# Kernel optimization log

Hardware: AMD Instinct MI355X
Metric: run time of the kernel (lower is better)

Reference implementation:

```python
import jax, jax.numpy as jnp
import numpy as np

B, C, H, W = 2, 320, 48, 48
HEADS, DIM_HEAD, NUM_FILTERS = 8, 64, 32
INNER = HEADS * DIM_HEAD  # 512
LN_EPS = 1e-05


def setup_inputs() -> dict:
    key = jax.random.key(0)
    ks = jax.random.split(key, 8)
    w = 0.02
    return {
        "hidden_states": jax.random.normal(ks[0], (B, C, H, W), jnp.float32),
        "encoder_hidden_states": jax.random.normal(ks[1], (B, C, H, W), jnp.float32),
        "Wq": jax.random.normal(ks[2], (C, INNER), jnp.float32) * w,
        "Wk": jax.random.normal(ks[3], (C, INNER), jnp.float32) * w,
        "Wv": jax.random.normal(ks[4], (C, INNER), jnp.float32) * w,
        "Wo": jax.random.normal(ks[5], (INNER, C), jnp.float32) * w,
        "bo": jnp.zeros((C,), jnp.float32),
        "ln_gamma": jnp.ones((C,), jnp.float32),
        "ln_beta": jnp.zeros((C,), jnp.float32),
        "ex_filters": jax.random.normal(ks[6], (NUM_FILTERS, INNER), jnp.float32),
        "dist_filters": jax.random.normal(ks[7], (NUM_FILTERS, INNER), jnp.float32),
        "scale": jnp.ones((1,), jnp.float32),  # learnable scale shadows dim_head**-0.5
    }


def _split_heads(t, heads):
    b, s, d = t.shape
    return t.reshape(b, s, heads, d // heads).transpose(0, 2, 1, 3)  # [b,h,s,dh]


def reference(hidden_states, encoder_hidden_states, Wq, Wk, Wv, Wo, bo,
              ln_gamma, ln_beta, ex_filters, dist_filters, scale):
    b, c, h, w = hidden_states.shape
    _, _, rh, rw = encoder_hidden_states.shape
    residual = hidden_states
    s = scale[0]

    hs = hidden_states.transpose(0, 2, 3, 1).reshape(b, h * w, c)        # [b, q, C]
    ehs = encoder_hidden_states.transpose(0, 2, 3, 1).reshape(b, rh * rw, c)

    # LayerNorm on encoder states
    mu = ehs.mean(-1, keepdims=True)
    var = jnp.mean((ehs - mu) ** 2, axis=-1, keepdims=True)
    ehs = (ehs - mu) * jax.lax.rsqrt(var + LN_EPS) * ln_gamma + ln_beta

    q = _split_heads(hs @ Wq, HEADS)    # [b,h,q,dh]
    k = _split_heads(ehs @ Wk, HEADS)   # [b,h,kv,dh]
    v = _split_heads(ehs @ Wv, HEADS)   # [b,h,kv,dh]
    ef = _split_heads(jnp.broadcast_to(ex_filters[None], (b,) + ex_filters.shape), HEADS)   # [b,h,F,dh]
    df = _split_heads(jnp.broadcast_to(dist_filters[None], (b,) + dist_filters.shape), HEADS)

    # spatial attention: softmax over kv positions
    spatial = jax.nn.softmax(jnp.einsum('bhfd,bhkd->bhfk', ef, k) * s, axis=-1)   # [b,h,F,kv]
    # channel attention: softmax over the filter axis (torch dim=1 of [B*h, F, q])
    channel = jax.nn.softmax(jnp.einsum('bhfd,bhqd->bhfq', df, q) * s, axis=2)    # [b,h,F,q]

    attn = jnp.einsum('bhfq,bhfk->bhqk', channel, spatial)                        # [b,h,q,kv]
    out = jnp.einsum('bhqk,bhkd->bhqd', attn, v)                                  # [b,h,q,dh]

    out = out.transpose(0, 2, 1, 3).reshape(b, h * w, INNER)
    out = out @ Wo + bo
    out = out.reshape(b, h, w, c).transpose(0, 3, 1, 2)
    return out + residual * s
```

## Files before the change

### kernel.cpp

```cpp
#include <hip/hip_runtime.h>
#include <math.h>

#define Bc 2
#define Cc 320
#define Pc 2304
#define HEADSc 8
#define DHc 64
#define INNERc 512
#define Fc 32
#define LN_EPS 1e-5f
#define CHUNKS 36
#define CHUNK_P 64

typedef __attribute__((ext_vector_type(8))) short bf16x8;
typedef __attribute__((ext_vector_type(4))) float f32x4;

static __device__ __forceinline__ ushort f2bf(float x) {
  uint u = __builtin_bit_cast(uint, x);
  u = (u + 0x7fffu + ((u >> 16) & 1u)) >> 16;
  return (ushort)u;
}

static __device__ __forceinline__ void gload16(const ushort* g, ushort* l) {
  __builtin_amdgcn_global_load_lds(
      (const __attribute__((address_space(1))) uint*)g,
      (__attribute__((address_space(3))) uint*)l, 16, 0, 0);
}

static __device__ void transpose_tile(const float* __restrict__ src,
                                      ushort* __restrict__ dst, int R, int C,
                                      int r0, int c0, int tid,
                                      float (*t)[65]) {
#pragma unroll
  for (int it = 0; it < 4; ++it) {
    int lin = it * 256 + tid;
    int rr = lin >> 4, c4 = lin & 15;
    float4 v = *(const float4*)(&src[(size_t)(r0 + rr) * C + c0 + c4 * 4]);
    t[rr][c4 * 4 + 0] = v.x; t[rr][c4 * 4 + 1] = v.y;
    t[rr][c4 * 4 + 2] = v.z; t[rr][c4 * 4 + 3] = v.w;
  }
  __syncthreads();
#pragma unroll
  for (int it = 0; it < 2; ++it) {
    int lin = it * 256 + tid;
    int cc = lin >> 3, r8 = lin & 7;
    ushort tmp[8];
#pragma unroll
    for (int j = 0; j < 8; ++j) tmp[j] = f2bf(t[r8 * 8 + j][cc]);
    *(uint4*)(&dst[(size_t)(c0 + cc) * R + r0 + r8 * 8]) = *(const uint4*)tmp;
  }
}

__global__ __launch_bounds__(256) void prep_all_kernel(
    const float* __restrict__ hs, const float* __restrict__ ehs,
    const float* __restrict__ gamma, const float* __restrict__ beta,
    const float* __restrict__ Wv, const float* __restrict__ Wo,
    const float* __restrict__ exf, const float* __restrict__ Wk,
    const float* __restrict__ dif, const float* __restrict__ Wq,
    ushort* __restrict__ hsT, ushort* __restrict__ ehsT,
    ushort* __restrict__ WvT, ushort* __restrict__ WoT,
    ushort* __restrict__ Gk, ushort* __restrict__ Gq) {
  __shared__ float smem[6448];
  int idx = blockIdx.x, tid = threadIdx.x;

  if (idx < 144) {
    int pt = idx % 36, z = idx / 36;
    int b = z & 1, which = z >> 1;
    int pos0 = pt * 64;
    const float* src = (which ? ehs : hs) + (size_t)b * Cc * Pc;
    ushort* dst = (which ? ehsT : hsT) + (size_t)b * Pc * Cc;
    float* t = smem;
    float* s1 = smem + 4160;
    float* s2 = smem + 4416;
    float* lmean = smem + 4672;
    float* lrstd = smem + 4736;
    int lane = tid & 63, g = tid >> 6;
    if (which) {
      const float* base = src + pos0 + lane;
      float sum = 0.f, sq = 0.f;
      for (int c = g * 80; c < g * 80 + 80; ++c) {
        float x = base[(size_t)c * Pc];
        sum += x; sq += x * x;
      }
      s1[g * 64 + lane] = sum; s2[g * 64 + lane] = sq;
      __syncthreads();
      if (tid < 64) {
        float ts = s1[tid] + s1[64 + tid] + s1[128 + tid] + s1[192 + tid];
        float tq = s2[tid] + s2[64 + tid] + s2[128 + tid] + s2[192 + tid];
        float mean = ts / (float)Cc;
        float var = tq / (float)Cc - mean * mean;
        lmean[tid] = mean;
        lrstd[tid] = rsqrtf(var + LN_EPS);
      }
      __syncthreads();
    }
    for (int ct = 0; ct < 5; ++ct) {
      int r0 = ct * 64;
#pragma unroll
      for (int it = 0; it < 4; ++it) {
        int lin = it * 256 + tid;
        int rr = lin >> 4, c4 = lin & 15;
        float4 v = *(const float4*)(&src[(size_t)(r0 + rr) * Pc + pos0 + c4 * 4]);
        t[rr * 65 + c4 * 4 + 0] = v.x; t[rr * 65 + c4 * 4 + 1] = v.y;
        t[rr * 65 + c4 * 4 + 2] = v.z; t[rr * 65 + c4 * 4 + 3] = v.w;
      }
      __syncthreads();
#pragma unroll
      for (int it = 0; it < 2; ++it) {
        int lin = it * 256 + tid;
        int cc = lin >> 3, r8 = lin & 7;
        float m_ = which ? lmean[cc] : 0.f, rs_ = which ? lrstd[cc] : 1.f;
        ushort tmp[8];
#pragma unroll
        for (int j = 0; j < 8; ++j) {
          int ch = r8 * 8 + j;
          float x = t[ch * 65 + cc];
          float val = which ? (x - m_) * rs_ * gamma[r0 + ch] + beta[r0 + ch] : x;
          tmp[j] = f2bf(val);
        }
        *(uint4*)(&dst[(size_t)(pos0 + cc) * Cc + r0 + r8 * 8]) =
            *(const uint4*)tmp;
      }
      __syncthreads();
    }
  } else {
    int idx2 = idx - 144;
    if (idx2 < 40) {
      transpose_tile(Wv, WvT, Cc, INNERc, (idx2 / 8) * 64, (idx2 % 8) * 64,
                     tid, (float(*)[65])smem);
    } else if (idx2 < 80) {
      int i = idx2 - 40;
      transpose_tile(Wo, WoT, INNERc, Cc, (i / 5) * 64, (i % 5) * 64, tid,
                     (float(*)[65])smem);
    } else {
      int i = idx2 - 80;
      int c0 = (i % 5) * 64, h = (i / 5) % 8, zz = i / 40;
      const float* filt = zz ? dif : exf;
      const float* W = zz ? Wq : Wk;
      ushort* G = zz ? Gq : Gk;
      float (*ef)[66] = (float(*)[66])smem;
      float (*wk)[65] = (float(*)[65])(smem + 32 * 66);
      for (int l = tid; l < Fc * DHc; l += 256) {
        int f = l >> 6, d = l & 63;
        ef[f][d] = filt[(size_t)f * INNERc + h * 64 + d];
      }
      for (int l = tid; l < 64 * DHc; l += 256) {
        int cc = l >> 6, d = l & 63;
        wk[cc][d] = W[(size_t)(c0 + cc) * INNERc + h * 64 + d];
      }
      __syncthreads();
      int f = tid >> 3, cbase = tid & 7;
      float acc[8] = {};
#pragma unroll
      for (int d4 = 0; d4 < DHc; d4 += 4) {
        float4 a = *(const float4*)(&ef[f][d4]);
#pragma unroll
        for (int j = 0; j < 8; ++j) {
          float4 b = *(const float4*)(&wk[cbase + j * 8][d4]);
          acc[j] += a.x * b.x + a.y * b.y + a.z * b.z + a.w * b.w;
        }
      }
#pragma unroll
      for (int j = 0; j < 8; ++j)
        G[(size_t)(h * Fc + f) * Cc + c0 + cbase + j * 8] = f2bf(acc[j]);
    }
  }
}

__global__ __launch_bounds__(256) void spatial_kernel(
    const ushort* __restrict__ Gk, const ushort* __restrict__ ehsT,
    const ushort* __restrict__ WvT, const float* __restrict__ scale_p,
    float* __restrict__ svp, float* __restrict__ mj, float* __restrict__ lj) {
  int c = blockIdx.x, h = blockIdx.y, b = blockIdx.z;
  int tid = threadIdx.x, lane = tid & 63, wv = tid >> 6;
  int l15 = lane & 15, kq = lane >> 4;
  int pos0 = c * CHUNK_P;
  int bh = b * HEADSc + h;
  float s = scale_p[0];

  __shared__ alignas(16) char smem[22528];
  ushort* As = (ushort*)smem;
  ushort* Bs = (ushort*)(smem + 12288);
  float* Sq = (float*)smem;
  ushort* Vs = (ushort*)(smem + 8704);
  ushort* P = (ushort*)(smem + 17920);

  const ushort* Av = WvT + (size_t)(h * 64) * Cc;
  const ushort* Ag = Gk + (size_t)(h * Fc) * Cc;
  const ushort* Bb = ehsT + ((size_t)b * Pc + pos0) * Cc;

  f32x4 acc[6] = {};
  for (int k0 = 0; k0 < Cc; k0 += 64) {
#pragma unroll
    for (int it = 0; it < 3; ++it) {
      int lin = it * 256 + tid;
      int row = lin >> 3, p = lin & 7;
      int lc = p ^ (row & 7);
      const ushort* sp = (row < 64) ? (Av + (size_t)row * Cc + k0 + lc * 8)
                                    : (Ag + (size_t)(row - 64) * Cc + k0 + lc * 8);
      gload16(sp, &As[lin * 8]);
    }
#pragma unroll
    for (int it = 0; it < 2; ++it) {
      int lin = it * 256 + tid;
      int row = lin >> 3, p = lin & 7;
      int lc = p ^ (row & 7);
      gload16(Bb + (size_t)row * Cc + k0 + lc * 8, &Bs[lin * 8]);
    }
    __syncthreads();
#pragma unroll
    for (int ss = 0; ss < 2; ++ss) {
      bf16x8 af[6], bfr;
#pragma unroll
      for (int mt = 0; mt < 6; ++mt) {
        int m = mt * 16 + l15;
        int p = (ss * 4 + kq) ^ (m & 7);
        af[mt] = *(const bf16x8*)(&As[m * 64 + p * 8]);
      }
      {
        int n = wv * 16 + l15;
        int p = (ss * 4 + kq) ^ (n & 7);
        bfr = *(const bf16x8*)(&Bs[n * 64 + p * 8]);
      }
#pragma unroll
      for (int mt = 0; mt < 6; ++mt)
        acc[mt] = __builtin_amdgcn_mfma_f32_16x16x32_bf16(af[mt], bfr, acc[mt],
                                                          0, 0, 0);
    }
    __syncthreads();
  }
#pragma unroll
  for (int mt = 0; mt < 6; ++mt) {
    int col = wv * 16 + l15;
#pragma unroll
    for (int r = 0; r < 4; ++r) {
      int row = mt * 16 + kq * 4 + r;
      if (mt < 4) Vs[row * 72 + col] = f2bf(acc[mt][r]);
      else Sq[(row - 64) * 68 + col] = acc[mt][r];
    }
  }
  __syncthreads();

  {
    int row = tid >> 3, sub = tid & 7;
    float vals[8];
    float m_ = -1e30f;
#pragma unroll
    for (int i = 0; i < 8; ++i) {
      vals[i] = s * Sq[row * 68 + sub * 8 + i];
      m_ = fmaxf(m_, vals[i]);
    }
    m_ = fmaxf(m_, __shfl_xor(m_, 1));
    m_ = fmaxf(m_, __shfl_xor(m_, 2));
    m_ = fmaxf(m_, __shfl_xor(m_, 4));
    float l_ = 0.f;
#pragma unroll
    for (int i = 0; i < 8; i += 2) {
      float e0 = __expf(vals[i] - m_);
      float e1 = __expf(vals[i + 1] - m_);
      l_ += e0 + e1;
      uint pk = (uint)f2bf(e0) | ((uint)f2bf(e1) << 16);
      *(uint*)(&P[row * 72 + sub * 8 + i]) = pk;
    }
    l_ += __shfl_xor(l_, 1);
    l_ += __shfl_xor(l_, 2);
    l_ += __shfl_xor(l_, 4);
    if (sub == 0) {
      mj[((size_t)c * 16 + bh) * Fc + row] = m_;
      lj[((size_t)c * 16 + bh) * Fc + row] = l_;
    }
  }
  __syncthreads();

  f32x4 acc2[2] = {};
#pragma unroll
  for (int ss = 0; ss < 2; ++ss) {
    bf16x8 af[2];
#pragma unroll
    for (int mt = 0; mt < 2; ++mt)
      af[mt] = *(const bf16x8*)(&P[(mt * 16 + l15) * 72 + ss * 32 + kq * 8]);
    bf16x8 bfr = *(const bf16x8*)(&Vs[(wv * 16 + l15) * 72 + ss * 32 + kq * 8]);
#pragma unroll
    for (int mt = 0; mt < 2; ++mt)
      acc2[mt] = __builtin_amdgcn_mfma_f32_16x16x32_bf16(af[mt], bfr, acc2[mt],
                                                         0, 0, 0);
  }
  float* op = svp + ((size_t)c * 16 + bh) * (Fc * DHc);
#pragma unroll
  for (int mt = 0; mt < 2; ++mt)
#pragma unroll
    for (int r = 0; r < 4; ++r)
      op[(mt * 16 + kq * 4 + r) * DHc + wv * 16 + l15] = acc2[mt][r];
}

__global__ __launch_bounds__(256) void sv_reduce_kernel(
    const float* __restrict__ svp, const float* __restrict__ mj,
    const float* __restrict__ lj, ushort* __restrict__ svT) {
  int idx = blockIdx.x * 256 + threadIdx.x;
  int d = idx & 63, fr = idx >> 6;
  int bh = fr >> 5, f = fr & 31;
  float m = -1e30f;
#pragma unroll
  for (int c = 0; c < CHUNKS; ++c)
    m = fmaxf(m, mj[((size_t)c * 16 + bh) * Fc + f]);
  float osum = 0.f, lsum = 0.f;
#pragma unroll 4
  for (int c = 0; c < CHUNKS; ++c) {
    float w = __expf(mj[((size_t)c * 16 + bh) * Fc + f] - m);
    osum += w * svp[((size_t)c * 16 + bh) * (Fc * DHc) + f * DHc + d];
    lsum += w * lj[((size_t)c * 16 + bh) * Fc + f];
  }
  svT[((size_t)bh * DHc + d) * Fc + f] = f2bf(osum / lsum);
}

__global__ __launch_bounds__(256) void channel_kernel(
    const ushort* __restrict__ Gq, const ushort* __restrict__ hsT,
    const ushort* __restrict__ svT, const float* __restrict__ scale_p,
    ushort* __restrict__ OAT) {
  int pb = blockIdx.x, h = blockIdx.y, b = blockIdx.z;
  int pos0 = pb * 64;
  int tid = threadIdx.x, lane = tid & 63, wv = tid >> 6;
  int l15 = lane & 15, kq = lane >> 4;
  float s = scale_p[0];

  __shared__ alignas(16) char smem[28672];
  ushort* Aq = (ushort*)smem;
  ushort* Bs = (ushort*)(smem + 4096);
  float* SO = (float*)smem;
  ushort* Pt = (ushort*)(smem + 17408);
  ushort* svs = (ushort*)(smem + 22528);
  float* red = (float*)(smem + 27648);

  f32x4 acc[2] = {};
  const ushort* Bb = hsT + ((size_t)b * Pc + pos0) * Cc;
  const ushort* Ab = Gq + (size_t)(h * Fc) * Cc;
  for (int k0 = 0; k0 < Cc; k0 += 64) {
    {
      int lin = tid;
      int row = lin >> 3, p = lin & 7;
      int lc = p ^ (row & 7);
      gload16(Ab + (size_t)row * Cc + k0 + lc * 8, &Aq[lin * 8]);
    }
#pragma unroll
    for (int it = 0; it < 2; ++it) {
      int lin = it * 256 + tid;
      int row = lin >> 3, p = lin & 7;
      int lc = p ^ (row & 7);
      gload16(Bb + (size_t)row * Cc + k0 + lc * 8, &Bs[lin * 8]);
    }
    __syncthreads();
#pragma unroll
    for (int ss = 0; ss < 2; ++ss) {
      int n = wv * 16 + l15;
      int pb_ = (ss * 4 + kq) ^ (n & 7);
      bf16x8 bfr = *(const bf16x8*)(&Bs[n * 64 + pb_ * 8]);
#pragma unroll
      for (int mt = 0; mt < 2; ++mt) {
        int m = mt * 16 + l15;
        int pa = (ss * 4 + kq) ^ (m & 7);
        bf16x8 af = *(const bf16x8*)(&Aq[m * 64 + pa * 8]);
        acc[mt] = __builtin_amdgcn_mfma_f32_16x16x32_bf16(af, bfr, acc[mt],
                                                          0, 0, 0);
      }
    }
    __syncthreads();
  }

#pragma unroll
  for (int mt = 0; mt < 2; ++mt)
#pragma unroll
    for (int r = 0; r < 4; ++r)
      SO[(mt * 16 + kq * 4 + r) * 68 + wv * 16 + l15] = acc[mt][r];
  {
    int rr = tid >> 2, p = tid & 3;
    *(uint4*)(&svs[rr * 40 + p * 8]) = *(const uint4*)(
        svT + ((size_t)(b * HEADSc + h) * DHc + rr) * Fc + p * 8);
  }
  __syncthreads();
  {
    int pos = tid & 63, g = tid >> 6;
    float v8[8];
    float pm = -1e30f;
#pragma unroll
    for (int i = 0; i < 8; ++i) {
      v8[i] = s * SO[(g * 8 + i) * 68 + pos];
      pm = fmaxf(pm, v8[i]);
    }
    red[g * 64 + pos] = pm;
    __syncthreads();
    float m_ = fmaxf(fmaxf(red[pos], red[64 + pos]),
                     fmaxf(red[128 + pos], red[192 + pos]));
    __syncthreads();
    float ps = 0.f;
#pragma unroll
    for (int i = 0; i < 8; ++i) {
      v8[i] = __expf(v8[i] - m_);
      ps += v8[i];
    }
    red[g * 64 + pos] = ps;
    __syncthreads();
    float inv = 1.f / (red[pos] + red[64 + pos] + red[128 + pos] +
                       red[192 + pos]);
#pragma unroll
    for (int i = 0; i < 8; i += 2) {
      uint pk = (uint)f2bf(v8[i] * inv) | ((uint)f2bf(v8[i + 1] * inv) << 16);
      *(uint*)(&Pt[pos * 40 + g * 8 + i]) = pk;
    }
  }
  __syncthreads();
  {
    bf16x8 b_ = *(const bf16x8*)(&svs[(wv * 16 + l15) * 40 + kq * 8]);
    f32x4 acc3[4];
#pragma unroll
    for (int mt = 0; mt < 4; ++mt) {
      bf16x8 a_ = *(const bf16x8*)(&Pt[(mt * 16 + l15) * 40 + kq * 8]);
      f32x4 z = {0.f, 0.f, 0.f, 0.f};
      acc3[mt] = __builtin_amdgcn_mfma_f32_16x16x32_bf16(a_, b_, z, 0, 0, 0);
    }
#pragma unroll
    for (int mt = 0; mt < 4; ++mt)
#pragma unroll
      for (int r = 0; r < 4; ++r)
        SO[(mt * 16 + kq * 4 + r) * 68 + wv * 16 + l15] = acc3[mt][r];
  }
  __syncthreads();
#pragma unroll
  for (int it = 0; it < 2; ++it) {
    int lin = it * 256 + tid;
    int p = lin >> 3, c8 = lin & 7;
    ushort tmp[8];
#pragma unroll
    for (int j = 0; j < 8; ++j) tmp[j] = f2bf(SO[p * 68 + c8 * 8 + j]);
    *(uint4*)(&OAT[((size_t)b * Pc + pos0 + p) * INNERc + h * 64 + c8 * 8]) =
        *(const uint4*)tmp;
  }
}

__global__ __launch_bounds__(256) void gemm_mfma_kernel(
    const ushort* __restrict__ A, const ushort* __restrict__ Bt,
    float* __restrict__ Out, int K, int Mdim,
    const float* __restrict__ bias, const float* __restrict__ res,
    const float* __restrict__ scale_p) {
  int b = blockIdx.z;
  int n0 = blockIdx.x * 64, m0 = blockIdx.y * 64;
  int tid = threadIdx.x, lane = tid & 63, wv = tid >> 6;
  int l15 = lane & 15, kq = lane >> 4;
  __shared__ alignas(16) ushort As[64 * 64];
  __shared__ alignas(16) ushort Bs[64 * 64];
  const ushort* Ab = A + (size_t)m0 * K;
  const ushort* Bb = Bt + ((size_t)b * Pc + n0) * K;

  f32x4 acc[4] = {};
  for (int k0 = 0; k0 < K; k0 += 64) {
#pragma unroll
    for (int it = 0; it < 2; ++it) {
      int lin = it * 256 + tid;
      int row = lin >> 3, p = lin & 7;
      int lc = p ^ (row & 7);
      gload16(Ab + (size_t)row * K + k0 + lc * 8, &As[lin * 8]);
    }
#pragma unroll
    for (int it = 0; it < 2; ++it) {
      int lin = it * 256 + tid;
      int row = lin >> 3, p = lin & 7;
      int lc = p ^ (row & 7);
      gload16(Bb + (size_t)row * K + k0 + lc * 8, &Bs[lin * 8]);
    }
    __syncthreads();
#pragma unroll
    for (int ss = 0; ss < 2; ++ss) {
      bf16x8 af[4], bfr;
#pragma unroll
      for (int mt = 0; mt < 4; ++mt) {
        int m = mt * 16 + l15;
        int p = (ss * 4 + kq) ^ (m & 7);
        af[mt] = *(const bf16x8*)(&As[m * 64 + p * 8]);
      }
      {
        int n = wv * 16 + l15;
        int p = (ss * 4 + kq) ^ (n & 7);
        bfr = *(const bf16x8*)(&Bs[n * 64 + p * 8]);
      }
#pragma unroll
      for (int mt = 0; mt < 4; ++mt)
        acc[mt] = __builtin_amdgcn_mfma_f32_16x16x32_bf16(af[mt], bfr, acc[mt],
                                                          0, 0, 0);
    }
    __syncthreads();
  }
  float s = scale_p[0];
  float* Ob = Out + ((size_t)b * Mdim + m0) * Pc + n0;
  const float* rb = res + ((size_t)b * Mdim + m0) * Pc + n0;
  int ncol = wv * 16 + l15;
#pragma unroll
  for (int mt = 0; mt < 4; ++mt)
#pragma unroll
    for (int r = 0; r < 4; ++r) {
      int m = mt * 16 + kq * 4 + r;
      Ob[(size_t)m * Pc + ncol] =
          acc[mt][r] + bias[m0 + m] + s * rb[(size_t)m * Pc + ncol];
    }
}

extern "C" void kernel_launch(void* const* d_in, const int* in_sizes, int n_in,
                              void* d_out, int out_size, void* d_ws, size_t ws_size,
                              hipStream_t stream) {
  const float* hs    = (const float*)d_in[0];
  const float* ehs   = (const float*)d_in[1];
  const float* Wq    = (const float*)d_in[2];
  const float* Wk    = (const float*)d_in[3];
  const float* Wv    = (const float*)d_in[4];
  const float* Wo    = (const float*)d_in[5];
  const float* bo    = (const float*)d_in[6];
  const float* gamma = (const float*)d_in[7];
  const float* beta  = (const float*)d_in[8];
  const float* exf   = (const float*)d_in[9];
  const float* dif   = (const float*)d_in[10];
  const float* scale = (const float*)d_in[11];
  float* out = (float*)d_out;

  float* ws = (float*)d_ws;
  float* svp = ws;
  float* mj  = svp + 1179648;
  float* lj  = mj + 18432;
  ushort* hsT  = (ushort*)(lj + 18432);
  ushort* ehsT = hsT + 1474560;
  ushort* WvT  = ehsT + 1474560;
  ushort* WoT  = WvT + 163840;
  ushort* Gk   = WoT + 163840;
  ushort* Gq   = Gk + 81920;
  ushort* svT  = Gq + 81920;
  ushort* OAT  = svT + 32768;

  prep_all_kernel<<<dim3(304), dim3(256), 0, stream>>>(
      hs, ehs, gamma, beta, Wv, Wo, exf, Wk, dif, Wq,
      hsT, ehsT, WvT, WoT, Gk, Gq);
  spatial_kernel<<<dim3(CHUNKS, HEADSc, Bc), dim3(256), 0, stream>>>(
      Gk, ehsT, WvT, scale, svp, mj, lj);
  sv_reduce_kernel<<<dim3(128), dim3(256), 0, stream>>>(svp, mj, lj, svT);
  channel_kernel<<<dim3(Pc / 64, HEADSc, Bc), dim3(256), 0, stream>>>(
      Gq, hsT, svT, scale, OAT);
  gemm_mfma_kernel<<<dim3(Pc / 64, Cc / 64, Bc), dim3(256), 0, stream>>>(
      WoT, OAT, out, INNERc, Cc, bo, hs, scale);
}
```

Baseline: 133.2 us.

## Double-buffer LDS tiles in MFMA GEMM kernels and prefetch transpose loads

Adds two-stage LDS double buffering to the spatial, channel and output-projection GEMM kernels, so the next K tile's async global-to-LDS loads are issued before the current tile's MFMAs run. The transpose/layernorm prep kernel also prefetches the next 64-channel slab into registers while the current slab is written out. The aim is to hide global memory latency behind compute. In exchange it raises LDS use (spatial kernel grows to 40KB), which may cut occupancy. The mid-loop barrier is removed, so correctness relies on the async LDS loads having completed by the trailing __syncthreads.

```diff
diff --git a/kernel.cpp b/kernel.cpp
--- a/kernel.cpp
+++ b/kernel.cpp
@@ -94,17 +94,31 @@
       }
       __syncthreads();
     }
+    float4 pv[4];
+#pragma unroll
+    for (int it = 0; it < 4; ++it) {
+      int lin = it * 256 + tid, rr = lin >> 4, c4 = lin & 15;
+      pv[it] = *(const float4*)(&src[(size_t)rr * Pc + pos0 + c4 * 4]);
+    }
     for (int ct = 0; ct < 5; ++ct) {
       int r0 = ct * 64;
 #pragma unroll
       for (int it = 0; it < 4; ++it) {
-        int lin = it * 256 + tid;
-        int rr = lin >> 4, c4 = lin & 15;
-        float4 v = *(const float4*)(&src[(size_t)(r0 + rr) * Pc + pos0 + c4 * 4]);
-        t[rr * 65 + c4 * 4 + 0] = v.x; t[rr * 65 + c4 * 4 + 1] = v.y;
-        t[rr * 65 + c4 * 4 + 2] = v.z; t[rr * 65 + c4 * 4 + 3] = v.w;
+        int lin = it * 256 + tid, rr = lin >> 4, c4 = lin & 15;
+        t[rr * 65 + c4 * 4 + 0] = pv[it].x;
+        t[rr * 65 + c4 * 4 + 1] = pv[it].y;
+        t[rr * 65 + c4 * 4 + 2] = pv[it].z;
+        t[rr * 65 + c4 * 4 + 3] = pv[it].w;
       }
       __syncthreads();
+      if (ct < 4) {
+#pragma unroll
+        for (int it = 0; it < 4; ++it) {
+          int lin = it * 256 + tid, rr = lin >> 4, c4 = lin & 15;
+          pv[it] =
+              *(const float4*)(&src[(size_t)(r0 + 64 + rr) * Pc + pos0 + c4 * 4]);
+        }
+      }
 #pragma unroll
       for (int it = 0; it < 2; ++it) {
         int lin = it * 256 + tid;
@@ -178,9 +192,7 @@
   int bh = b * HEADSc + h;
   float s = scale_p[0];
 
-  __shared__ alignas(16) char smem[22528];
-  ushort* As = (ushort*)smem;
-  ushort* Bs = (ushort*)(smem + 12288);
+  __shared__ alignas(16) char smem[40960];
   float* Sq = (float*)smem;
   ushort* Vs = (ushort*)(smem + 8704);
   ushort* P = (ushort*)(smem + 17920);
@@ -189,25 +201,36 @@
   const ushort* Ag = Gk + (size_t)(h * Fc) * Cc;
   const ushort* Bb = ehsT + ((size_t)b * Pc + pos0) * Cc;
 
-  f32x4 acc[6] = {};
-  for (int k0 = 0; k0 < Cc; k0 += 64) {
+  auto stage = [&](int buf, int k0) {
+    ushort* As_ = (ushort*)(smem + buf * 20480);
+    ushort* Bs_ = (ushort*)(smem + buf * 20480 + 12288);
 #pragma unroll
     for (int it = 0; it < 3; ++it) {
       int lin = it * 256 + tid;
       int row = lin >> 3, p = lin & 7;
       int lc = p ^ (row & 7);
-      const ushort* sp = (row < 64) ? (Av + (size_t)row * Cc + k0 + lc * 8)
-                                    : (Ag + (size_t)(row - 64) * Cc + k0 + lc * 8);
-      gload16(sp, &As[lin * 8]);
+      const ushort* sp = (row < 64)
+                             ? (Av + (size_t)row * Cc + k0 + lc * 8)
+                             : (Ag + (size_t)(row - 64) * Cc + k0 + lc * 8);
+      gload16(sp, &As_[lin * 8]);
     }
 #pragma unroll
     for (int it = 0; it < 2; ++it) {
       int lin = it * 256 + tid;
       int row = lin >> 3, p = lin & 7;
       int lc = p ^ (row & 7);
-      gload16(Bb + (size_t)row * Cc + k0 + lc * 8, &Bs[lin * 8]);
-    }
-    __syncthreads();
+      gload16(Bb + (size_t)row * Cc + k0 + lc * 8, &Bs_[lin * 8]);
+    }
+  };
+
+  f32x4 acc[6] = {};
+  stage(0, 0);
+  __syncthreads();
+  int cur = 0;
+  for (int t = 0; t < 5; ++t) {
+    if (t < 4) stage(cur ^ 1, (t + 1) * 64);
+    const ushort* As_ = (const ushort*)(smem + cur * 20480);
+    const ushort* Bs_ = (const ushort*)(smem + cur * 20480 + 12288);
 #pragma unroll
     for (int ss = 0; ss < 2; ++ss) {
       bf16x8 af[6], bfr;
@@ -215,12 +238,12 @@
       for (int mt = 0; mt < 6; ++mt) {
         int m = mt * 16 + l15;
         int p = (ss * 4 + kq) ^ (m & 7);
-        af[mt] = *(const bf16x8*)(&As[m * 64 + p * 8]);
+        af[mt] = *(const bf16x8*)(&As_[m * 64 + p * 8]);
       }
       {
         int n = wv * 16 + l15;
         int p = (ss * 4 + kq) ^ (n & 7);
-        bfr = *(const bf16x8*)(&Bs[n * 64 + p * 8]);
+        bfr = *(const bf16x8*)(&Bs_[n * 64 + p * 8]);
       }
 #pragma unroll
       for (int mt = 0; mt < 6; ++mt)
@@ -228,6 +251,7 @@
                                                           0, 0, 0);
     }
     __syncthreads();
+    cur ^= 1;
   }
 #pragma unroll
   for (int mt = 0; mt < 6; ++mt) {
@@ -324,46 +348,54 @@
   float s = scale_p[0];
 
   __shared__ alignas(16) char smem[28672];
-  ushort* Aq = (ushort*)smem;
-  ushort* Bs = (ushort*)(smem + 4096);
   float* SO = (float*)smem;
   ushort* Pt = (ushort*)(smem + 17408);
   ushort* svs = (ushort*)(smem + 22528);
   float* red = (float*)(smem + 27648);
 
-  f32x4 acc[2] = {};
   const ushort* Bb = hsT + ((size_t)b * Pc + pos0) * Cc;
   const ushort* Ab = Gq + (size_t)(h * Fc) * Cc;
-  for (int k0 = 0; k0 < Cc; k0 += 64) {
+
+  auto stage = [&](int buf, int k0) {
+    ushort* Aq_ = (ushort*)(smem + buf * 12288);
+    ushort* Bs_ = (ushort*)(smem + buf * 12288 + 4096);
     {
-      int lin = tid;
-      int row = lin >> 3, p = lin & 7;
+      int lin = tid, row = lin >> 3, p = lin & 7;
       int lc = p ^ (row & 7);
-      gload16(Ab + (size_t)row * Cc + k0 + lc * 8, &Aq[lin * 8]);
+      gload16(Ab + (size_t)row * Cc + k0 + lc * 8, &Aq_[lin * 8]);
     }
 #pragma unroll
     for (int it = 0; it < 2; ++it) {
-      int lin = it * 256 + tid;
-      int row = lin >> 3, p = lin & 7;
+      int lin = it * 256 + tid, row = lin >> 3, p = lin & 7;
       int lc = p ^ (row & 7);
-      gload16(Bb + (size_t)row * Cc + k0 + lc * 8, &Bs[lin * 8]);
-    }
-    __syncthreads();
+      gload16(Bb + (size_t)row * Cc + k0 + lc * 8, &Bs_[lin * 8]);
+    }
+  };
+
+  f32x4 acc[2] = {};
+  stage(0, 0);
+  __syncthreads();
+  int cur = 0;
+  for (int t = 0; t < 5; ++t) {
+    if (t < 4) stage(cur ^ 1, (t + 1) * 64);
+    const ushort* Aq_ = (const ushort*)(smem + cur * 12288);
+    const ushort* Bs_ = (const ushort*)(smem + cur * 12288 + 4096);
 #pragma unroll
     for (int ss = 0; ss < 2; ++ss) {
       int n = wv * 16 + l15;
       int pb_ = (ss * 4 + kq) ^ (n & 7);
-      bf16x8 bfr = *(const bf16x8*)(&Bs[n * 64 + pb_ * 8]);
+      bf16x8 bfr = *(const bf16x8*)(&Bs_[n * 64 + pb_ * 8]);
 #pragma unroll
       for (int mt = 0; mt < 2; ++mt) {
         int m = mt * 16 + l15;
         int pa = (ss * 4 + kq) ^ (m & 7);
-        bf16x8 af = *(const bf16x8*)(&Aq[m * 64 + pa * 8]);
+        bf16x8 af = *(const bf16x8*)(&Aq_[m * 64 + pa * 8]);
         acc[mt] = __builtin_amdgcn_mfma_f32_16x16x32_bf16(af, bfr, acc[mt],
                                                           0, 0, 0);
       }
     }
     __syncthreads();
+    cur ^= 1;
   }
 
 #pragma unroll
@@ -445,28 +477,36 @@
   int n0 = blockIdx.x * 64, m0 = blockIdx.y * 64;
   int tid = threadIdx.x, lane = tid & 63, wv = tid >> 6;
   int l15 = lane & 15, kq = lane >> 4;
-  __shared__ alignas(16) ushort As[64 * 64];
-  __shared__ alignas(16) ushort Bs[64 * 64];
+  __shared__ alignas(16) char smem[32768];
   const ushort* Ab = A + (size_t)m0 * K;
   const ushort* Bb = Bt + ((size_t)b * Pc + n0) * K;
 
+  auto stage = [&](int buf, int k0) {
+    ushort* As_ = (ushort*)(smem + buf * 16384);
+    ushort* Bs_ = (ushort*)(smem + buf * 16384 + 8192);
+#pragma unroll
+    for (int it = 0; it < 2; ++it) {
+      int lin = it * 256 + tid, row = lin >> 3, p = lin & 7;
+      int lc = p ^ (row & 7);
+      gload16(Ab + (size_t)row * K + k0 + lc * 8, &As_[lin * 8]);
+    }
+#pragma unroll
+    for (int it = 0; it < 2; ++it) {
+      int lin = it * 256 + tid, row = lin >> 3, p = lin & 7;
+      int lc = p ^ (row & 7);
+      gload16(Bb + (size_t)row * K + k0 + lc * 8, &Bs_[lin * 8]);
+    }
+  };
+
   f32x4 acc[4] = {};
-  for (int k0 = 0; k0 < K; k0 += 64) {
-#pragma unroll
-    for (int it = 0; it < 2; ++it) {
-      int lin = it * 256 + tid;
-      int row = lin >> 3, p = lin & 7;
-      int lc = p ^ (row & 7);
-      gload16(Ab + (size_t)row * K + k0 + lc * 8, &As[lin * 8]);
-    }
-#pragma unroll
-    for (int it = 0; it < 2; ++it) {
-      int lin = it * 256 + tid;
-      int row = lin >> 3, p = lin & 7;
-      int lc = p ^ (row & 7);
-      gload16(Bb + (size_t)row * K + k0 + lc * 8, &Bs[lin * 8]);
-    }
-    __syncthreads();
+  stage(0, 0);
+  __syncthreads();
+  int cur = 0;
+  const int NT = K >> 6;
+  for (int t = 0; t < NT; ++t) {
+    if (t < NT - 1) stage(cur ^ 1, (t + 1) * 64);
+    const ushort* As_ = (const ushort*)(smem + cur * 16384);
+    const ushort* Bs_ = (const ushort*)(smem + cur * 16384 + 8192);
 #pragma unroll
     for (int ss = 0; ss < 2; ++ss) {
       bf16x8 af[4], bfr;
@@ -474,12 +514,12 @@
       for (int mt = 0; mt < 4; ++mt) {
         int m = mt * 16 + l15;
         int p = (ss * 4 + kq) ^ (m & 7);
-        af[mt] = *(const bf16x8*)(&As[m * 64 + p * 8]);
+        af[mt] = *(const bf16x8*)(&As_[m * 64 + p * 8]);
       }
       {
         int n = wv * 16 + l15;
         int p = (ss * 4 + kq) ^ (n & 7);
-        bfr = *(const bf16x8*)(&Bs[n * 64 + p * 8]);
+        bfr = *(const bf16x8*)(&Bs_[n * 64 + p * 8]);
       }
 #pragma unroll
       for (int mt = 0; mt < 4; ++mt)
@@ -487,6 +527,7 @@
                                                           0, 0, 0);
     }
     __syncthreads();
+    cur ^= 1;
   }
   float s = scale_p[0];
   float* Ob = Out + ((size_t)b * Mdim + m0) * Pc + n0;
```

Result: no change. 132.1 us (median of 2 runs) (-0.8%).
